# Performance work log

Hardware: AMD Instinct MI355X
Metric: run time of the kernel (lower is better)

## Reference

```python
import jax, jax.numpy as jnp
import numpy as np

E = 8  # moe_num_experts


def setup_inputs() -> dict:
    key = jax.random.key(0)
    ks = jax.random.split(key, 6)
    T, H, F, K = 8192, 768, 3072, 2
    x = jax.random.normal(ks[0], (T, H), dtype=jnp.float32)
    weights = jax.random.uniform(ks[1], (T, E), dtype=jnp.float32)
    top_weights = jax.random.uniform(ks[2], (T, K), dtype=jnp.float32)
    top_experts = jax.random.randint(ks[3], (T, K), 0, E)
    w1 = jax.random.normal(ks[4], (E, F, H), dtype=jnp.float32) * 0.02
    w2 = jax.random.normal(ks[5], (E, F, H), dtype=jnp.float32) * 0.02
    bias = jnp.zeros((H,), dtype=jnp.float32)
    return {"x": x, "weights": weights, "top_weights": top_weights,
            "top_experts": top_experts, "w1": w1, "w2": w2, "bias": bias}


def reference(x, weights, top_weights, top_experts, w1, w2, bias):
    # combine[t, e] = sum_k top_weights[t, k] * 1[top_experts[t, k] == e]
    one_hot = jax.nn.one_hot(top_experts, E, dtype=x.dtype)  # [T, K, E]
    combine = jnp.einsum('tke,tk->te', one_hot, top_weights)  # [T, E]
    out = jnp.zeros_like(x)
    for e in range(E):  # fixed small expert loop
        h = jax.nn.gelu(x @ w1[e].T, approximate=False)  # [T, F]
        out = out + (h @ w2[e]) * combine[:, e:e + 1]
    return out + bias
```

## Files before the change

### kernel.cpp

```cpp
#include <hip/hip_runtime.h>
#include <math.h>

#define TT   8192
#define HH   768
#define FF   3072
#define NEXP 8
#define NP   16384
#define BM   128
#define BM1  256
#define MTP1 72
#define ESTR (FF*HH)

typedef unsigned short u16;
typedef __attribute__((ext_vector_type(8))) short bf16x8;
typedef __attribute__((ext_vector_type(4))) float f32x4;

__device__ __forceinline__ u16 f2b(float f) {
  unsigned u = __float_as_uint(f);
  unsigned r = (u + 0x7FFFu + ((u >> 16) & 1u)) >> 16;
  return (u16)r;
}

__device__ __forceinline__ float b2f(u16 b) {
  return __uint_as_float(((unsigned)b) << 16);
}

__device__ __forceinline__ float gelu_fast(float v) {
  float u  = v * (0.7978845608f + 0.0356774081f * v * v);
  float ex = __expf(2.0f * u);
  float th = 1.0f - 2.0f * __builtin_amdgcn_rcpf(ex + 1.0f);
  return 0.5f * v * (1.0f + th);
}

__device__ __forceinline__ float gelu_exact(float v) {
  return 0.5f * v * (1.0f + erff(v * 0.70710678118654752f));
}

__device__ __forceinline__ void gll16(const void* g, void* l) {
  __builtin_amdgcn_global_load_lds(
      (const __attribute__((address_space(1))) void*)g,
      (__attribute__((address_space(3))) void*)l, 16, 0, 0);
}

__global__ __launch_bounds__(1024)
void route_all(const int* __restrict__ te, const float* __restrict__ tw,
               int* __restrict__ hdr) {
  __shared__ int cnt[NEXP], cur[NEXP];
  const int tid = threadIdx.x;
  const int lane = tid & 63, wave = tid >> 6;
  if (tid < NEXP) cnt[tid] = 0;
  __syncthreads();
  for (int base = wave * 64; base < NP; base += 1024) {
    int e = te[base + lane];
#pragma unroll
    for (int x = 0; x < NEXP; ++x) {
      unsigned long long m = __ballot(e == x);
      if (lane == 0 && m) atomicAdd(&cnt[x], __popcll(m));
    }
  }
  __syncthreads();
  if (tid == 0) {
    int run = 0, t2 = 0;
#pragma unroll
    for (int x = 0; x < NEXP; ++x) {
      cur[x] = run;
      hdr[x] = cnt[x]; hdr[16 + x] = run;
      run += cnt[x];
    }
    for (int x = 0; x < NEXP; ++x) {
      int n2 = (cnt[x] + BM1 - 1) >> 8;
      for (int i = 0; i < n2; ++i) { hdr[49504 + t2] = x; hdr[49576 + t2] = i * BM1; ++t2; }
    }
    hdr[9] = t2;
  }
  __syncthreads();
  for (int base = wave * 64; base < NP; base += 1024) {
    int i = base + lane;
    int e = te[i];
    float w = tw[i];
    int slot = 0;
#pragma unroll
    for (int x = 0; x < NEXP; ++x) {
      unsigned long long m = __ballot(e == x);
      int nb = __popcll(m);
      int below = __popcll(m & ((1ull << lane) - 1ull));
      int b = 0;
      if (lane == 0) b = nb ? atomicAdd(&cur[x], nb) : 0;
      b = __shfl(b, 0);
      if (e == x) slot = b + below;
    }
    hdr[352 + slot] = i >> 1;
    ((float*)(hdr + 16736))[slot] = w;
    hdr[33120 + i] = slot;
  }
}

__global__ void cvt_all(const float* __restrict__ x, const float* __restrict__ w1,
                        u16* __restrict__ dst, int xn4, int totn4) {
  for (int i = blockIdx.x * 256 + threadIdx.x; i < totn4; i += gridDim.x * 256) {
    float4 v = (i < xn4) ? ((const float4*)x)[i] : ((const float4*)w1)[i - xn4];
    ushort4 o;
    o.x = f2b(v.x); o.y = f2b(v.y); o.z = f2b(v.z); o.w = f2b(v.w);
    ((ushort4*)dst)[i] = o;
  }
}

__global__ void transpose_w2(const float* __restrict__ w2, u16* __restrict__ w2t) {
  __shared__ u16 t[64][65];
  int e = blockIdx.z;
  int f0 = blockIdx.x * 64, h0 = blockIdx.y * 64;
  int tid = threadIdx.x;
  int tx = tid & 15, ty = tid >> 4;
  const float* s = w2 + (size_t)e * ESTR;
#pragma unroll
  for (int j = 0; j < 4; ++j) {
    int f = f0 + ty + 16 * j;
    float4 v = *(const float4*)&s[(size_t)f * HH + h0 + tx * 4];
    t[ty + 16 * j][tx * 4 + 0] = f2b(v.x);
    t[ty + 16 * j][tx * 4 + 1] = f2b(v.y);
    t[ty + 16 * j][tx * 4 + 2] = f2b(v.z);
    t[ty + 16 * j][tx * 4 + 3] = f2b(v.w);
  }
  __syncthreads();
  u16* d = w2t + (size_t)e * ESTR;
#pragma unroll
  for (int j = 0; j < 4; ++j) {
    int hr = ty + 16 * j;
    ushort4 o;
    o.x = t[tx * 4 + 0][hr];
    o.y = t[tx * 4 + 1][hr];
    o.z = t[tx * 4 + 2][hr];
    o.w = t[tx * 4 + 3][hr];
    *(ushort4*)&d[(size_t)(h0 + hr) * FF + f0 + tx * 4] = o;
  }
}

__global__ void bias_init(float* __restrict__ out, const float* __restrict__ bias) {
  int i = blockIdx.x * 256 + threadIdx.x;
  if (i < TT * HH / 4)
    ((float4*)out)[i] = ((const float4*)bias)[i % (HH / 4)];
}

__global__ void combine(const u16* __restrict__ part, const int* __restrict__ hdr,
                        const float* __restrict__ bias, float* __restrict__ out) {
  int t = blockIdx.x;
  int c = threadIdx.x;
  const int* inv = hdr + 33120;
  const float* pw = (const float*)(hdr + 16736);
  int g0 = inv[2 * t], g1 = inv[2 * t + 1];
  float w0 = pw[g0], w1 = pw[g1];
  ushort4 p0 = ((const ushort4*)(part + (size_t)g0 * HH))[c];
  ushort4 p1 = ((const ushort4*)(part + (size_t)g1 * HH))[c];
  float4 b  = ((const float4*)bias)[c];
  float4 o;
  o.x = b.x + w0 * b2f(p0.x) + w1 * b2f(p1.x);
  o.y = b.y + w0 * b2f(p0.y) + w1 * b2f(p1.y);
  o.z = b.z + w0 * b2f(p0.z) + w1 * b2f(p1.z);
  o.w = b.w + w0 * b2f(p0.w) + w1 * b2f(p1.w);
  ((float4*)(out + (size_t)t * HH))[c] = o;
}

template <int PHASE, int NT, int G>
__global__ __launch_bounds__(512, 4)
void moe_gemm(const u16* __restrict__ Asrc, const u16* __restrict__ Bsrc,
              u16* __restrict__ Outp, const int* __restrict__ hdr) {
  constexpr int KEXT = (PHASE == 1) ? HH : FF;
  constexpr int AST  = (PHASE == 1) ? HH : FF;
  constexpr int BST  = (PHASE == 1) ? HH : FF;
  constexpr int OST  = (PHASE == 1) ? FF : HH;
  constexpr int NK   = KEXT / 32;

  const int nwg = NT * MTP1;
  const int bid = blockIdx.x;
  const int l   = (bid & 7) * (nwg >> 3) + (bid >> 3);
  const int mtl = l % G;
  const int nt  = (l / G) % NT;
  const int sg  = l / (G * NT);
  const int mt  = sg * G + mtl;
  if (mt >= hdr[9]) return;

  const int e   = hdr[49504 + mt];
  const int m0  = hdr[49576 + mt];
  const int cnt = hdr[e];
  const int off = hdr[16 + e];
  const int* ptok = hdr + 352;

  __shared__ u16 Al[3][8192];
  __shared__ u16 Bl[3][4096];

  const int tid  = threadIdx.x;
  const int lane = tid & 63;
  const int wave = tid >> 6;
  const int wm = wave >> 1, wn = wave & 1;
  const int lr = lane & 15;

  const int kcs = (((tid & 3) ^ ((tid >> 3) & 3)) * 8);
  const u16* aptr[2];
#pragma unroll
  for (int i = 0; i < 2; ++i) {
    int r = (tid >> 2) + 128 * i;
    int g = off + m0 + r; g = g < NP ? g : NP - 1;
    if (PHASE == 1)
      aptr[i] = Asrc + (size_t)ptok[g] * AST + kcs;
    else
      aptr[i] = Asrc + (size_t)g * AST + kcs;
  }
  const u16* bptr = Bsrc + (size_t)e * ESTR +
                    (size_t)(nt * BM + (tid >> 2)) * BST + kcs;

  f32x4 acc[4][4] = {};
  const int pcs = (((lane >> 4) ^ ((lane >> 1) & 3)) * 8);

#define STG(BS, T) do {                                   \
    gll16(aptr[0] + (T) * 32, &Al[BS][tid * 8]);          \
    gll16(aptr[1] + (T) * 32, &Al[BS][tid * 8 + 4096]);   \
    gll16(bptr + (T) * 32, &Bl[BS][tid * 8]);             \
  } while (0)

#define ITER(BC, BS, TSTG, DOST, VMN) do {                                   \
    asm volatile("s_waitcnt vmcnt(" #VMN ")" ::: "memory");                  \
    __builtin_amdgcn_sched_barrier(0);                                       \
    __builtin_amdgcn_s_barrier();                                            \
    bf16x8 af[4], bfr[4];                                                    \
    _Pragma("unroll")                                                        \
    for (int i = 0; i < 4; ++i)                                              \
      af[i] = *(const bf16x8*)&Al[BC][(wm * 64 + i * 16 + lr) * 32 + pcs];   \
    _Pragma("unroll")                                                        \
    for (int i = 0; i < 4; ++i)                                              \
      bfr[i] = *(const bf16x8*)&Bl[BC][(wn * 64 + i * 16 + lr) * 32 + pcs];  \
    if (DOST) STG(BS, TSTG);                                                 \
    asm volatile("s_waitcnt lgkmcnt(0)" ::: "memory");                       \
    __builtin_amdgcn_sched_barrier(0);                                       \
    __builtin_amdgcn_s_setprio(1);                                           \
    _Pragma("unroll")                                                        \
    for (int mi = 0; mi < 4; ++mi)                                           \
      _Pragma("unroll")                                                      \
      for (int ni = 0; ni < 4; ++ni)                                         \
        acc[mi][ni] = __builtin_amdgcn_mfma_f32_16x16x32_bf16(               \
            af[mi], bfr[ni], acc[mi][ni], 0, 0, 0);                          \
    __builtin_amdgcn_s_setprio(0);                                           \
  } while (0)

  STG(0, 0);
  STG(1, 1);

  for (int g = 0; g < NK / 3 - 1; ++g) {
    const int t0 = g * 3;
    ITER(0, 2, t0 + 2, 1, 3);
    ITER(1, 0, t0 + 3, 1, 3);
    ITER(2, 1, t0 + 4, 1, 3);
  }
  ITER(0, 2, NK - 1, 1, 3);
  ITER(1, 0, 0, 0, 3);
  ITER(2, 0, 0, 0, 0);
#undef ITER
#undef STG

#pragma unroll
  for (int mi = 0; mi < 4; ++mi)
#pragma unroll
    for (int ni = 0; ni < 4; ++ni)
#pragma unroll
      for (int j = 0; j < 4; ++j) {
        int rl = wm * 64 + mi * 16 + (lane >> 4) * 4 + j;
        int gr = m0 + rl;
        if (gr < cnt) {
          int col = nt * BM + wn * 64 + ni * 16 + lr;
          float v = acc[mi][ni][j];
          if (PHASE == 1) v = gelu_fast(v);
          Outp[(size_t)(off + gr) * OST + col] = f2b(v);
        }
      }
}

__global__ void naive_pair(const float* __restrict__ x, const float* __restrict__ tw,
                           const int* __restrict__ te, const float* __restrict__ w1,
                           const float* __restrict__ w2, float* __restrict__ out) {
  __shared__ float xs[HH];
  __shared__ float hb[FF];
  int t = blockIdx.x >> 1, k = blockIdx.x & 1;
  int e = te[t * 2 + k];
  float wt = tw[t * 2 + k];
  for (int i = threadIdx.x; i < HH; i += 256) xs[i] = x[(size_t)t * HH + i];
  __syncthreads();
  const float* W1 = w1 + (size_t)e * ESTR;
  for (int f = threadIdx.x; f < FF; f += 256) {
    float s = 0.f;
    const float* r = W1 + (size_t)f * HH;
    for (int i = 0; i < HH; ++i) s += xs[i] * r[i];
    hb[f] = gelu_exact(s);
  }
  __syncthreads();
  const float* W2 = w2 + (size_t)e * ESTR;
  for (int c = threadIdx.x; c < HH; c += 256) {
    float s = 0.f;
    for (int f = 0; f < FF; ++f) s += hb[f] * W2[(size_t)f * HH + c];
    atomicAdd(&out[(size_t)t * HH + c], s * wt);
  }
}

extern "C" void kernel_launch(void* const* d_in, const int* in_sizes, int n_in,
                              void* d_out, int out_size, void* d_ws, size_t ws_size,
                              hipStream_t stream) {
  const float* x    = (const float*)d_in[0];
  const float* topw = (const float*)d_in[2];
  const int*   tope = (const int*)d_in[3];
  const float* w1   = (const float*)d_in[4];
  const float* w2   = (const float*)d_in[5];
  const float* bias = (const float*)d_in[6];
  float* out = (float*)d_out;

  char* ws = (char*)d_ws;
  const size_t HDRB   = 1u << 18;
  const size_t xb_off  = HDRB;
  const size_t xb_sz   = (size_t)TT * HH * 2;
  const size_t w1_off  = xb_off + xb_sz;
  const size_t w1_sz   = (size_t)NEXP * ESTR * 2;
  const size_t w2t_off = w1_off + w1_sz;
  const size_t w2t_sz  = w1_sz;
  const size_t h_off   = w2t_off + w2t_sz;
  const size_t h_sz    = (size_t)NP * FF * 2;
  const size_t need    = h_off + h_sz;

  if (ws_size < need) {
    bias_init<<<(TT * HH / 4 + 255) / 256, 256, 0, stream>>>(out, bias);
    naive_pair<<<NP, 256, 0, stream>>>(x, topw, tope, w1, w2, out);
    return;
  }

  int* hdr   = (int*)ws;
  u16* xb    = (u16*)(ws + xb_off);
  u16* w1b   = (u16*)(ws + w1_off);
  u16* w2t   = (u16*)(ws + w2t_off);
  u16* h     = (u16*)(ws + h_off);
  u16* part  = (u16*)(ws + xb_off);

  route_all<<<1, 1024, 0, stream>>>(tope, topw, hdr);

  const int XN4 = TT * HH / 4;
  const int TOTN4 = (TT * HH + NEXP * ESTR) / 4;
  cvt_all<<<2048, 256, 0, stream>>>(x, w1, xb, XN4, TOTN4);
  transpose_w2<<<dim3(FF / 64, HH / 64, NEXP), 256, 0, stream>>>(w2, w2t);

  moe_gemm<1, 24, 8><<<24 * MTP1, 512, 0, stream>>>(xb, w1b, h, hdr);
  moe_gemm<2, 6, 2><<<6 * MTP1, 512, 0, stream>>>(h, w2t, part, hdr);
  combine<<<TT, HH / 4, 0, stream>>>(part, hdr, bias, out);
}
```

Baseline: 309.1 us.

## Split phase-1 GEMM into dedicated 256x256-tile kernel with ping-pong K pipeline

The first expert GEMM (x·W1 with gelu) moves to its own kernel. It uses 256x256 output tiles, 64-wide K steps split into two 32-wide halves, and double-buffered LDS. Staging of A and B for the next step is interleaved with the MFMA phases, with s_setprio raised around the MFMA blocks, and occupancy drops to 2 workgroups per CU. The goal is more arithmetic intensity per LDS and global load for the dominant first GEMM, at the cost of more registers and LDS and fewer workgroups in flight. The second GEMM keeps its old schedule, specialised into its own kernel.

Measured after the change: 329.4 us. 6.6% more time.

```diff
diff --git a/kernel.cpp b/kernel.cpp
--- a/kernel.cpp
+++ b/kernel.cpp
@@ -160,16 +160,11 @@
   ((float4*)(out + (size_t)t * HH))[c] = o;
 }
 
-template <int PHASE, int NT, int G>
-__global__ __launch_bounds__(512, 4)
-void moe_gemm(const u16* __restrict__ Asrc, const u16* __restrict__ Bsrc,
-              u16* __restrict__ Outp, const int* __restrict__ hdr) {
-  constexpr int KEXT = (PHASE == 1) ? HH : FF;
-  constexpr int AST  = (PHASE == 1) ? HH : FF;
-  constexpr int BST  = (PHASE == 1) ? HH : FF;
-  constexpr int OST  = (PHASE == 1) ? FF : HH;
-  constexpr int NK   = KEXT / 32;
-
+template <int NT, int G>
+__global__ __launch_bounds__(512, 2)
+void moe_gemm1p(const u16* __restrict__ Asrc, const u16* __restrict__ Bsrc,
+                u16* __restrict__ Hout, const int* __restrict__ hdr) {
+  constexpr int NK = HH / 64;
   const int nwg = NT * MTP1;
   const int bid = blockIdx.x;
   const int l   = (bid & 7) * (nwg >> 3) + (bid >> 3);
@@ -185,6 +180,134 @@
   const int off = hdr[16 + e];
   const int* ptok = hdr + 352;
 
+  __shared__ u16 Al[2][2][8192];
+  __shared__ u16 Bl[2][2][8192];
+
+  const int tid  = threadIdx.x;
+  const int lane = tid & 63;
+  const int wave = tid >> 6;
+  const int wm = wave >> 2, wn = wave & 3;
+  const int lr = lane & 15;
+
+  const int kcs = (((tid & 3) ^ ((tid >> 3) & 3)) * 8);
+  const u16* aptr[2];
+  const u16* bptr[2];
+#pragma unroll
+  for (int i = 0; i < 2; ++i) {
+    int r = i * 128 + (tid >> 2);
+    int g = off + m0 + r; g = g < NP ? g : NP - 1;
+    aptr[i] = Asrc + (size_t)ptok[g] * HH + kcs;
+    int br = nt * 256 + r;
+    bptr[i] = Bsrc + (size_t)e * ESTR + (size_t)br * HH + kcs;
+  }
+
+  f32x4 acc[8][4] = {};
+  bf16x8 bfr[4];
+  const int pcs = (((lane >> 4) ^ ((lane >> 1) & 3)) * 8);
+
+#define SA(BUF, H, T) do {                                         \
+    gll16(aptr[0] + (T) * 64 + (H) * 32, &Al[BUF][H][tid * 8]);    \
+    gll16(aptr[1] + (T) * 64 + (H) * 32, &Al[BUF][H][4096 + tid * 8]); \
+  } while (0)
+#define SB(BUF, H, T) do {                                         \
+    gll16(bptr[0] + (T) * 64 + (H) * 32, &Bl[BUF][H][tid * 8]);    \
+    gll16(bptr[1] + (T) * 64 + (H) * 32, &Bl[BUF][H][4096 + tid * 8]); \
+  } while (0)
+
+#define WAITB(N) do {                                              \
+    asm volatile("s_waitcnt vmcnt(" #N ")" ::: "memory");          \
+    __builtin_amdgcn_sched_barrier(0);                             \
+    __builtin_amdgcn_s_barrier();                                  \
+    __builtin_amdgcn_sched_barrier(0);                             \
+  } while (0)
+
+#define PHB(BUF, KK, MH, DOB, SSEL, SH, ST) {                                \
+    bf16x8 af[4];                                                            \
+    if (DOB) {                                                               \
+      _Pragma("unroll")                                                      \
+      for (int ni = 0; ni < 4; ++ni) {                                       \
+        int rr = wn * 64 + ni * 16 + lr;                                     \
+        bfr[ni] = *(const bf16x8*)&Bl[BUF][KK][rr * 32 + pcs];               \
+      }                                                                      \
+    }                                                                        \
+    _Pragma("unroll")                                                        \
+    for (int q = 0; q < 4; ++q) {                                            \
+      int rr = wm * 128 + ((MH) * 4 + q) * 16 + lr;                          \
+      af[q] = *(const bf16x8*)&Al[BUF][KK][rr * 32 + pcs];                   \
+    }                                                                        \
+    if (SSEL == 1) SA((BUF) ^ 1, SH, ST);                                    \
+    else if (SSEL == 2) SB((BUF) ^ 1, SH, ST);                               \
+    asm volatile("s_waitcnt lgkmcnt(0)" ::: "memory");                       \
+    __builtin_amdgcn_sched_barrier(0);                                       \
+    __builtin_amdgcn_s_setprio(1);                                           \
+    _Pragma("unroll")                                                        \
+    for (int q = 0; q < 4; ++q)                                              \
+      _Pragma("unroll")                                                      \
+      for (int ni = 0; ni < 4; ++ni)                                         \
+        acc[(MH) * 4 + q][ni] = __builtin_amdgcn_mfma_f32_16x16x32_bf16(     \
+            af[q], bfr[ni], acc[(MH) * 4 + q][ni], 0, 0, 0);                 \
+    __builtin_amdgcn_s_setprio(0);                                           \
+  }
+
+  SA(0, 0, 0); SB(0, 0, 0); SA(0, 1, 0); SB(0, 1, 0);
+
+  for (int t = 0; t < NK - 1; ++t) {
+    const int buf = t & 1;
+    WAITB(4);
+    PHB(buf, 0, 0, 1, 1, 0, t + 1);
+    PHB(buf, 0, 1, 0, 2, 0, t + 1);
+    WAITB(4);
+    PHB(buf, 1, 0, 1, 1, 1, t + 1);
+    PHB(buf, 1, 1, 0, 2, 1, t + 1);
+  }
+  {
+    const int buf = (NK - 1) & 1;
+    WAITB(4);
+    PHB(buf, 0, 0, 1, 0, 0, 0);
+    PHB(buf, 0, 1, 0, 0, 0, 0);
+    WAITB(0);
+    PHB(buf, 1, 0, 1, 0, 0, 0);
+    PHB(buf, 1, 1, 0, 0, 0, 0);
+  }
+#undef PHB
+#undef WAITB
+#undef SB
+#undef SA
+
+#pragma unroll
+  for (int mi = 0; mi < 8; ++mi)
+#pragma unroll
+    for (int ni = 0; ni < 4; ++ni)
+#pragma unroll
+      for (int j = 0; j < 4; ++j) {
+        int rl = wm * 128 + mi * 16 + (lane >> 4) * 4 + j;
+        int gr = m0 + rl;
+        if (gr < cnt) {
+          int col = nt * 256 + wn * 64 + ni * 16 + lr;
+          Hout[(size_t)(off + gr) * FF + col] = f2b(gelu_fast(acc[mi][ni][j]));
+        }
+      }
+}
+
+template <int NT, int G>
+__global__ __launch_bounds__(512, 4)
+void moe_gemm2(const u16* __restrict__ Asrc, const u16* __restrict__ Bsrc,
+               u16* __restrict__ Outp, const int* __restrict__ hdr) {
+  constexpr int NK = FF / 32;
+  const int nwg = NT * MTP1;
+  const int bid = blockIdx.x;
+  const int l   = (bid & 7) * (nwg >> 3) + (bid >> 3);
+  const int mtl = l % G;
+  const int nt  = (l / G) % NT;
+  const int sg  = l / (G * NT);
+  const int mt  = sg * G + mtl;
+  if (mt >= hdr[9]) return;
+
+  const int e   = hdr[49504 + mt];
+  const int m0  = hdr[49576 + mt];
+  const int cnt = hdr[e];
+  const int off = hdr[16 + e];
+
   __shared__ u16 Al[3][8192];
   __shared__ u16 Bl[3][4096];
 
@@ -200,13 +323,10 @@
   for (int i = 0; i < 2; ++i) {
     int r = (tid >> 2) + 128 * i;
     int g = off + m0 + r; g = g < NP ? g : NP - 1;
-    if (PHASE == 1)
-      aptr[i] = Asrc + (size_t)ptok[g] * AST + kcs;
-    else
-      aptr[i] = Asrc + (size_t)g * AST + kcs;
+    aptr[i] = Asrc + (size_t)g * FF + kcs;
   }
   const u16* bptr = Bsrc + (size_t)e * ESTR +
-                    (size_t)(nt * BM + (tid >> 2)) * BST + kcs;
+                    (size_t)(nt * BM + (tid >> 2)) * FF + kcs;
 
   f32x4 acc[4][4] = {};
   const int pcs = (((lane >> 4) ^ ((lane >> 1) & 3)) * 8);
@@ -266,9 +386,7 @@
         int gr = m0 + rl;
         if (gr < cnt) {
           int col = nt * BM + wn * 64 + ni * 16 + lr;
-          float v = acc[mi][ni][j];
-          if (PHASE == 1) v = gelu_fast(v);
-          Outp[(size_t)(off + gr) * OST + col] = f2b(v);
+          Outp[(size_t)(off + gr) * HH + col] = f2b(acc[mi][ni][j]);
         }
       }
 }
@@ -342,7 +460,7 @@
   cvt_all<<<2048, 256, 0, stream>>>(x, w1, xb, XN4, TOTN4);
   transpose_w2<<<dim3(FF / 64, HH / 64, NEXP), 256, 0, stream>>>(w2, w2t);
 
-  moe_gemm<1, 24, 8><<<24 * MTP1, 512, 0, stream>>>(xb, w1b, h, hdr);
-  moe_gemm<2, 6, 2><<<6 * MTP1, 512, 0, stream>>>(h, w2t, part, hdr);
+  moe_gemm1p<12, 8><<<12 * MTP1, 512, 0, stream>>>(xb, w1b, h, hdr);
+  moe_gemm2<6, 2><<<6 * MTP1, 512, 0, stream>>>(h, w2t, part, hdr);
   combine<<<TT, HH / 4, 0, stream>>>(part, hdr, bias, out);
 }
```

## Split-K the second expert GEMM into two partial buffers summed in combine

Applied to the files above, without the earlier changes.

The down-projection GEMM (K=3072) is split into two K halves, each launched as a separate workgroup that writes bf16 partials to its own buffer. The combine kernel now reads and sums both partial buffers per routed token before applying the routing weights and bias. The aim is to double the workgroup count for the phase-2 GEMM so the GPU is better filled and each workgroup runs a shorter K loop. In exchange it doubles the partial-output writes and combine reads, and adds one extra bf16 rounding step before the final sum.

Measured after the change: 312.4 us. No clear change (+1.1%).

```diff
diff --git a/kernel.cpp b/kernel.cpp
--- a/kernel.cpp
+++ b/kernel.cpp
@@ -149,35 +149,41 @@
   const float* pw = (const float*)(hdr + 16736);
   int g0 = inv[2 * t], g1 = inv[2 * t + 1];
   float w0 = pw[g0], w1 = pw[g1];
-  ushort4 p0 = ((const ushort4*)(part + (size_t)g0 * HH))[c];
-  ushort4 p1 = ((const ushort4*)(part + (size_t)g1 * HH))[c];
+  const u16* pk0 = part;
+  const u16* pk1 = part + (size_t)NP * HH;
+  ushort4 a0 = ((const ushort4*)(pk0 + (size_t)g0 * HH))[c];
+  ushort4 a1 = ((const ushort4*)(pk1 + (size_t)g0 * HH))[c];
+  ushort4 b0 = ((const ushort4*)(pk0 + (size_t)g1 * HH))[c];
+  ushort4 b1 = ((const ushort4*)(pk1 + (size_t)g1 * HH))[c];
   float4 b  = ((const float4*)bias)[c];
   float4 o;
-  o.x = b.x + w0 * b2f(p0.x) + w1 * b2f(p1.x);
-  o.y = b.y + w0 * b2f(p0.y) + w1 * b2f(p1.y);
-  o.z = b.z + w0 * b2f(p0.z) + w1 * b2f(p1.z);
-  o.w = b.w + w0 * b2f(p0.w) + w1 * b2f(p1.w);
+  o.x = b.x + w0 * (b2f(a0.x) + b2f(a1.x)) + w1 * (b2f(b0.x) + b2f(b1.x));
+  o.y = b.y + w0 * (b2f(a0.y) + b2f(a1.y)) + w1 * (b2f(b0.y) + b2f(b1.y));
+  o.z = b.z + w0 * (b2f(a0.z) + b2f(a1.z)) + w1 * (b2f(b0.z) + b2f(b1.z));
+  o.w = b.w + w0 * (b2f(a0.w) + b2f(a1.w)) + w1 * (b2f(b0.w) + b2f(b1.w));
   ((float4*)(out + (size_t)t * HH))[c] = o;
 }
 
-template <int PHASE, int NT, int G>
+template <int PHASE, int NT, int G, int KS>
 __global__ __launch_bounds__(512, 4)
 void moe_gemm(const u16* __restrict__ Asrc, const u16* __restrict__ Bsrc,
               u16* __restrict__ Outp, const int* __restrict__ hdr) {
-  constexpr int KEXT = (PHASE == 1) ? HH : FF;
+  constexpr int KEXT = (PHASE == 1) ? HH : (FF / KS);
   constexpr int AST  = (PHASE == 1) ? HH : FF;
   constexpr int BST  = (PHASE == 1) ? HH : FF;
   constexpr int OST  = (PHASE == 1) ? FF : HH;
   constexpr int NK   = KEXT / 32;
 
-  const int nwg = NT * MTP1;
+  const int nwg = NT * MTP1 * KS;
   const int bid = blockIdx.x;
   const int l   = (bid & 7) * (nwg >> 3) + (bid >> 3);
   const int mtl = l % G;
   const int nt  = (l / G) % NT;
-  const int sg  = l / (G * NT);
+  const int kg  = (l / (G * NT)) % KS;
+  const int sg  = l / (G * NT * KS);
   const int mt  = sg * G + mtl;
   if (mt >= hdr[9]) return;
+  const int kbase = kg * KEXT;
 
   const int e   = hdr[49504 + mt];
   const int m0  = hdr[49576 + mt];
@@ -203,10 +209,10 @@
     if (PHASE == 1)
       aptr[i] = Asrc + (size_t)ptok[g] * AST + kcs;
     else
-      aptr[i] = Asrc + (size_t)g * AST + kcs;
+      aptr[i] = Asrc + (size_t)g * AST + kbase + kcs;
   }
   const u16* bptr = Bsrc + (size_t)e * ESTR +
-                    (size_t)(nt * BM + (tid >> 2)) * BST + kcs;
+                    (size_t)(nt * BM + (tid >> 2)) * BST + kbase + kcs;
 
   f32x4 acc[4][4] = {};
   const int pcs = (((lane >> 4) ^ ((lane >> 1) & 3)) * 8);
@@ -256,6 +262,7 @@
 #undef ITER
 #undef STG
 
+  u16* outb = Outp + (PHASE == 1 ? 0 : (size_t)kg * NP * HH);
 #pragma unroll
   for (int mi = 0; mi < 4; ++mi)
 #pragma unroll
@@ -268,7 +275,7 @@
           int col = nt * BM + wn * 64 + ni * 16 + lr;
           float v = acc[mi][ni][j];
           if (PHASE == 1) v = gelu_fast(v);
-          Outp[(size_t)(off + gr) * OST + col] = f2b(v);
+          outb[(size_t)(off + gr) * OST + col] = f2b(v);
         }
       }
 }
@@ -342,7 +349,7 @@
   cvt_all<<<2048, 256, 0, stream>>>(x, w1, xb, XN4, TOTN4);
   transpose_w2<<<dim3(FF / 64, HH / 64, NEXP), 256, 0, stream>>>(w2, w2t);
 
-  moe_gemm<1, 24, 8><<<24 * MTP1, 512, 0, stream>>>(xb, w1b, h, hdr);
-  moe_gemm<2, 6, 2><<<6 * MTP1, 512, 0, stream>>>(h, w2t, part, hdr);
+  moe_gemm<1, 24, 8, 1><<<24 * MTP1, 512, 0, stream>>>(xb, w1b, h, hdr);
+  moe_gemm<2, 6, 2, 2><<<6 * MTP1 * 2, 512, 0, stream>>>(h, w2t, part, hdr);
   combine<<<TT, HH / 4, 0, stream>>>(part, hdr, bias, out);
 }
```
